# Kernel optimization log

Hardware: AMD Instinct MI355X
Metric: run time of the kernel (lower is better)

Reference implementation:

```python
import jax, jax.numpy as jnp
import numpy as np

EMBED_DIM = 1024
ATTN_DIM = 128
B, S = 4, 2048


def setup_inputs() -> dict:
    key = jax.random.key(0)
    k1, k2, k3, k4 = jax.random.split(key, 4)
    embedded = jax.random.normal(k1, (B, S, EMBED_DIM), dtype=jnp.float32)
    # torch nn.Linear weights are [out_features, in_features]
    scale = 1.0 / np.sqrt(EMBED_DIM)
    Wk = jax.random.uniform(k2, (ATTN_DIM, EMBED_DIM), dtype=jnp.float32, minval=-scale, maxval=scale)
    Wq = jax.random.uniform(k3, (ATTN_DIM, EMBED_DIM), dtype=jnp.float32, minval=-scale, maxval=scale)
    Wv = jax.random.uniform(k4, (ATTN_DIM, EMBED_DIM), dtype=jnp.float32, minval=-scale, maxval=scale)
    return {"embedded": embedded, "Wk": Wk, "Wq": Wq, "Wv": Wv}


def reference(embedded, Wk, Wq, Wv):
    # projections (no bias): x @ W.T
    k = jnp.einsum('bse,ae->bsa', embedded, Wk)  # [B,S,A]
    q = jnp.einsum('bse,ae->bsa', embedded, Wq)
    v = jnp.einsum('bse,ae->bsa', embedded, Wv)
    ad = k.shape[-1]
    scores = jnp.einsum('bqa,bka->bqk', q, k) / jnp.sqrt(jnp.float32(ad))  # [B,S,S]
    causal = jnp.tril(jnp.ones((scores.shape[1], scores.shape[1]), dtype=bool))
    scores = jnp.where(causal, scores, -jnp.inf)
    probs = jax.nn.softmax(scores, axis=-1)
    out = jnp.einsum('bqk,bka->bqa', probs, v)
    return jnp.round(out, 4)
```

## Files before the change

kernel.cpp:

```cpp
#include <hip/hip_runtime.h>
#include <hip/hip_bf16.h>
#include <math.h>

#define B 4
#define S 2048
#define E 1024
#define A 128
#define CHUNK 256
#define NCHMAX 8

typedef __attribute__((ext_vector_type(8))) short short8;
typedef __attribute__((ext_vector_type(4))) float floatx4;

static __device__ __forceinline__ short f2bf(float f) {
  union { float f; unsigned u; } c;
  c.f = f;
  unsigned r = (c.u + 0x7fffu + ((c.u >> 16) & 1u)) >> 16;
  return (short)r;
}
static __device__ __forceinline__ unsigned f2bf2(float x, float y) {
  __hip_bfloat162 h = __float22bfloat162_rn(float2{x, y});
  union { __hip_bfloat162 h; unsigned u; } c;
  c.h = h;
  return c.u;
}

__global__ __launch_bounds__(256) void wconv(
    const float* __restrict__ Wq,
    const float* __restrict__ Wk,
    const float* __restrict__ Wv,
    short* __restrict__ Wbf) {
  const int which = blockIdx.y;
  const float* Wp = (which == 0) ? Wq : (which == 1) ? Wk : Wv;
  short* o = Wbf + (size_t)which * A * E;
  const int f = blockIdx.x * 256 + threadIdx.x;
  const float4 v = *(const float4*)&Wp[(size_t)f * 4];
  uint2 p; p.x = f2bf2(v.x, v.y); p.y = f2bf2(v.z, v.w);
  *(uint2*)&o[(size_t)f * 4] = p;
}

#define PJ 72
__global__ __launch_bounds__(256) void proj_gemm(
    const float* __restrict__ X,
    const short* __restrict__ Wbf,
    short* __restrict__ Qbf,
    short* __restrict__ Kbf,
    short* __restrict__ Vt) {
  __shared__ short As[64 * PJ];
  __shared__ short Bs[128 * PJ];

  const int m0 = blockIdx.x * 64;
  const int which = blockIdx.y;
  const short* Wpb = Wbf + (size_t)which * A * E;

  const int tid = threadIdx.x;
  const int wave = tid >> 6;
  const int lane = tid & 63;
  const int mh = wave & 1;
  const int nh = wave >> 1;
  const int l16 = lane & 15;
  const int quad = lane >> 4;

  int arow[4], ac4[4], brow[4], bc8[4];
#pragma unroll
  for (int i = 0; i < 4; ++i) {
    const int fa = tid + i * 256;
    arow[i] = fa >> 4; ac4[i] = fa & 15;
    const int fb = tid + i * 256;
    brow[i] = fb >> 3; bc8[i] = fb & 7;
  }

  floatx4 acc[2][4] = {};
  float4 aplf[4];
  short8 bplf[4];

#pragma unroll
  for (int i = 0; i < 4; ++i) {
    aplf[i] = *(const float4*)&X[(size_t)(m0 + arow[i]) * E + ac4[i] * 4];
    bplf[i] = *(const short8*)&Wpb[(size_t)brow[i] * E + bc8[i] * 8];
  }

  for (int k0 = 0; k0 < E; k0 += 64) {
    __syncthreads();
#pragma unroll
    for (int i = 0; i < 4; ++i) {
      uint2 p; p.x = f2bf2(aplf[i].x, aplf[i].y); p.y = f2bf2(aplf[i].z, aplf[i].w);
      *(uint2*)&As[arow[i] * PJ + ac4[i] * 4] = p;
      *(short8*)&Bs[brow[i] * PJ + bc8[i] * 8] = bplf[i];
    }
    __syncthreads();

    if (k0 + 64 < E) {
#pragma unroll
      for (int i = 0; i < 4; ++i) {
        aplf[i] = *(const float4*)&X[(size_t)(m0 + arow[i]) * E + (k0 + 64) + ac4[i] * 4];
        bplf[i] = *(const short8*)&Wpb[(size_t)brow[i] * E + (k0 + 64) + bc8[i] * 8];
      }
    }

    short8 afr[2][2], bfr[4][2];
#pragma unroll
    for (int ms = 0; ms < 2; ++ms)
#pragma unroll
      for (int ks = 0; ks < 2; ++ks)
        afr[ms][ks] = *(const short8*)&As[(mh * 32 + ms * 16 + l16) * PJ + ks * 32 + quad * 8];
#pragma unroll
    for (int nt = 0; nt < 4; ++nt)
#pragma unroll
      for (int ks = 0; ks < 2; ++ks)
        bfr[nt][ks] = *(const short8*)&Bs[(nh * 64 + nt * 16 + l16) * PJ + ks * 32 + quad * 8];

#pragma unroll
    for (int ms = 0; ms < 2; ++ms)
#pragma unroll
      for (int nt = 0; nt < 4; ++nt)
#pragma unroll
        for (int ks = 0; ks < 2; ++ks)
          acc[ms][nt] = __builtin_amdgcn_mfma_f32_16x16x32_bf16(
              afr[ms][ks], bfr[nt][ks], acc[ms][nt], 0, 0, 0);
  }

  const float qscale = 0.08838834764831845f;
#pragma unroll
  for (int ms = 0; ms < 2; ++ms) {
#pragma unroll
    for (int nt = 0; nt < 4; ++nt) {
      const int n = nh * 64 + nt * 16 + l16;
      const int mbase = m0 + mh * 32 + ms * 16 + quad * 4;
      if (which == 2) {
        const int b = mbase >> 11, s = mbase & (S - 1);
        short4 p;
        p.x = f2bf(acc[ms][nt][0]); p.y = f2bf(acc[ms][nt][1]);
        p.z = f2bf(acc[ms][nt][2]); p.w = f2bf(acc[ms][nt][3]);
        *(short4*)&Vt[((size_t)b * A + n) * S + s] = p;
      } else {
        short* Outp = (which == 0) ? Qbf : Kbf;
        const float sc = (which == 0) ? qscale : 1.0f;
#pragma unroll
        for (int r = 0; r < 4; ++r)
          Outp[(size_t)(mbase + r) * A + n] = f2bf(acc[ms][nt][r] * sc);
      }
    }
  }
}

#define LK 132
#define LV 68
__global__ __launch_bounds__(256) void attn_part(
    const short* __restrict__ Qbf,
    const short* __restrict__ Kbf,
    const short* __restrict__ Vt,
    float* __restrict__ Opart,
    float* __restrict__ Lpart) {
  __shared__ short Ks[64 * LK];
  __shared__ short Vs[128 * LV];
  __shared__ short Ps[4][16 * LV];

  const int rev = (int)gridDim.x - 1 - (int)blockIdx.x;
  const int qt = rev >> 3;
  const int chunk = rev & 7;
  const int b = qt >> 5;
  const int q0 = (qt & 31) << 6;
  const int nk = q0 + 64;
  const int kstart = chunk * CHUNK;
  if (kstart >= nk) return;
  const int kend = min(kstart + CHUNK, nk);

  const int tid = threadIdx.x;
  const int wave = tid >> 6;
  const int lane = tid & 63;
  const int l16 = lane & 15;
  const int quad = lane >> 4;

  int krow[4], kc8[4], vrow[4], vc8[4];
#pragma unroll
  for (int i = 0; i < 4; ++i) {
    const int f = tid + i * 256;
    krow[i] = f >> 4; kc8[i] = f & 15;
    vrow[i] = f >> 3; vc8[i] = f & 7;
  }

  short8 qfr[4];
  {
    const size_t qrow = (size_t)(b * S + q0 + wave * 16 + l16);
#pragma unroll
    for (int ks = 0; ks < 4; ++ks)
      qfr[ks] = *(const short8*)&Qbf[qrow * A + ks * 32 + quad * 8];
  }

  float l_acc[4] = {0.f, 0.f, 0.f, 0.f};
  floatx4 oacc[8] = {};

  const int myrow = q0 + wave * 16 + quad * 4;
  const short* Kbase = Kbf + (size_t)b * S * A;
  const short* Vbase = Vt + (size_t)b * A * S;

  short8 kplf[4], vplf[4];
#pragma unroll
  for (int i = 0; i < 4; ++i) {
    kplf[i] = *(const short8*)&Kbase[(size_t)(kstart + krow[i]) * A + kc8[i] * 8];
    vplf[i] = *(const short8*)&Vbase[(size_t)vrow[i] * S + kstart + vc8[i] * 8];
  }

  for (int j0 = kstart; j0 < kend; j0 += 64) {
    __syncthreads();
#pragma unroll
    for (int i = 0; i < 4; ++i) {
      *(short8*)&Ks[krow[i] * LK + kc8[i] * 8] = kplf[i];
      *(short8*)&Vs[vrow[i] * LV + vc8[i] * 8] = vplf[i];
    }
    __syncthreads();

    if (j0 + 64 < kend) {
#pragma unroll
      for (int i = 0; i < 4; ++i) {
        kplf[i] = *(const short8*)&Kbase[(size_t)(j0 + 64 + krow[i]) * A + kc8[i] * 8];
        vplf[i] = *(const short8*)&Vbase[(size_t)vrow[i] * S + j0 + 64 + vc8[i] * 8];
      }
    }

    floatx4 sc[4];
#pragma unroll
    for (int nt = 0; nt < 4; ++nt) {
      floatx4 c = {};
#pragma unroll
      for (int ks = 0; ks < 4; ++ks) {
        const short8 bfr = *(const short8*)&Ks[(nt * 16 + l16) * LK + ks * 32 + quad * 8];
        c = __builtin_amdgcn_mfma_f32_16x16x32_bf16(qfr[ks], bfr, c, 0, 0, 0);
      }
      sc[nt] = c;
    }

#pragma unroll
    for (int nt = 0; nt < 4; ++nt) {
      const int key = j0 + nt * 16 + l16;
#pragma unroll
      for (int r = 0; r < 4; ++r) {
        const float p = (key > myrow + r) ? 0.f : __expf(sc[nt][r]);
        sc[nt][r] = p;
        l_acc[r] += p;
      }
    }

#pragma unroll
    for (int nt = 0; nt < 4; ++nt)
#pragma unroll
      for (int r = 0; r < 4; ++r)
        Ps[wave][(quad * 4 + r) * LV + nt * 16 + l16] = f2bf(sc[nt][r]);

    short8 pfr[2];
#pragma unroll
    for (int ks = 0; ks < 2; ++ks)
      pfr[ks] = *(const short8*)&Ps[wave][l16 * LV + ks * 32 + quad * 8];

#pragma unroll
    for (int nt = 0; nt < 8; ++nt) {
#pragma unroll
      for (int ks = 0; ks < 2; ++ks) {
        const short8 vfr = *(const short8*)&Vs[(nt * 16 + l16) * LV + ks * 32 + quad * 8];
        oacc[nt] = __builtin_amdgcn_mfma_f32_16x16x32_bf16(pfr[ks], vfr, oacc[nt], 0, 0, 0);
      }
    }
  }

  const int slot = qt * NCHMAX + chunk;
  float* op = Opart + (size_t)slot * 64 * 128;
  const int lr = wave * 16 + quad * 4;
#pragma unroll
  for (int nt = 0; nt < 8; ++nt)
#pragma unroll
    for (int r = 0; r < 4; ++r)
      op[(lr + r) * 128 + nt * 16 + l16] = oacc[nt][r];

#pragma unroll
  for (int r = 0; r < 4; ++r) {
    float l = l_acc[r];
    l += __shfl_xor(l, 1);
    l += __shfl_xor(l, 2);
    l += __shfl_xor(l, 4);
    l += __shfl_xor(l, 8);
    if (l16 == 0) Lpart[slot * 64 + lr + r] = l;
  }
}

__global__ __launch_bounds__(256) void attn_reduce(
    const float* __restrict__ Opart,
    const float* __restrict__ Lpart,
    float* __restrict__ Out) {
  const int qt = blockIdx.x;
  const int b = qt >> 5;
  const int q0 = (qt & 31) << 6;
  const int nch = (q0 + 64 + CHUNK - 1) / CHUNK;

  const int tid = threadIdx.x;
  const int lr = tid >> 2;
  const int c0 = (tid & 3) * 32;

  float ltot = 0.f;
  for (int c = 0; c < nch; ++c) ltot += Lpart[(qt * NCHMAX + c) * 64 + lr];
  const float inv = 1.f / ltot;

  float4 acc[8] = {};
  for (int c = 0; c < nch; ++c) {
    const float4* op = (const float4*)
        (Opart + ((size_t)(qt * NCHMAX + c) * 64 + lr) * 128 + c0);
#pragma unroll
    for (int i = 0; i < 8; ++i) {
      const float4 v = op[i];
      acc[i].x += v.x; acc[i].y += v.y; acc[i].z += v.z; acc[i].w += v.w;
    }
  }

  float4* o = (float4*)(Out + (size_t)(b * S + q0 + lr) * A + c0);
#pragma unroll
  for (int i = 0; i < 8; ++i) {
    float4 v = acc[i];
    v.x *= inv; v.y *= inv; v.z *= inv; v.w *= inv;
    o[i] = v;
  }
}

extern "C" void kernel_launch(void* const* d_in, const int* in_sizes, int n_in,
                              void* d_out, int out_size, void* d_ws, size_t ws_size,
                              hipStream_t stream) {
  const float* X  = (const float*)d_in[0];
  const float* Wk = (const float*)d_in[1];
  const float* Wq = (const float*)d_in[2];
  const float* Wv = (const float*)d_in[3];
  float* Out = (float*)d_out;

  const size_t qkv_elems = (size_t)B * S * A;
  short* Qbf = (short*)d_ws;
  short* Kbf = Qbf + qkv_elems;
  short* Vt  = Kbf + qkv_elems;
  float* Opart = (float*)(Vt + qkv_elems);
  float* Lpart = Opart + (size_t)1024 * 64 * 128;
  short* Wbf = (short*)(Lpart + (size_t)1024 * 64);

  wconv<<<dim3(A * E / 4 / 256, 3), 256, 0, stream>>>(Wq, Wk, Wv, Wbf);
  dim3 pgrid(B * S / 64, 3);
  proj_gemm<<<pgrid, 256, 0, stream>>>(X, Wbf, Qbf, Kbf, Vt);
  attn_part<<<(B * S / 64) * NCHMAX, 256, 0, stream>>>(Qbf, Kbf, Vt, Opart, Lpart);
  attn_reduce<<<B * S / 64, 256, 0, stream>>>(Opart, Lpart, Out);
}
```

Before: 129.9 us.

## XOR-swizzle LDS tiles, double-prefetch projection loads, split reduce blocks

Replaces padded LDS row strides with XOR-swizzled unpadded layouts for the projection GEMM tiles and the attention K/V tiles, aiming to avoid bank conflicts while using less shared memory. The projection GEMM now keeps two register prefetch buffers in flight, loading two K-steps ahead to hide global latency. Address arithmetic is precomputed outside the loops. The reduce kernel launches twice as many blocks, each handling half the rows, to improve occupancy. The extra prefetch buffers raise register pressure in the projection kernel.

```diff
diff --git a/kernel.cpp b/kernel.cpp
--- a/kernel.cpp
+++ b/kernel.cpp
@@ -39,15 +39,14 @@
   *(uint2*)&o[(size_t)f * 4] = p;
 }
 
-#define PJ 72
 __global__ __launch_bounds__(256) void proj_gemm(
     const float* __restrict__ X,
     const short* __restrict__ Wbf,
     short* __restrict__ Qbf,
     short* __restrict__ Kbf,
     short* __restrict__ Vt) {
-  __shared__ short As[64 * PJ];
-  __shared__ short Bs[128 * PJ];
+  __shared__ short As[64 * 64];
+  __shared__ short Bs[128 * 64];
 
   const int m0 = blockIdx.x * 64;
   const int which = blockIdx.y;
@@ -61,64 +60,74 @@
   const int l16 = lane & 15;
   const int quad = lane >> 4;
 
-  int arow[4], ac4[4], brow[4], bc8[4];
+  int xbase[4], wbase[4], aoff[4], boff[4];
 #pragma unroll
   for (int i = 0; i < 4; ++i) {
     const int fa = tid + i * 256;
-    arow[i] = fa >> 4; ac4[i] = fa & 15;
+    const int arow = fa >> 4, ac4 = fa & 15;
+    xbase[i] = (m0 + arow) * E + ac4 * 4;
+    aoff[i] = arow * 64 + (((ac4 >> 1) ^ (arow & 7)) << 3) + ((ac4 & 1) << 2);
     const int fb = tid + i * 256;
-    brow[i] = fb >> 3; bc8[i] = fb & 7;
-  }
+    const int brow = fb >> 3, bc8 = fb & 7;
+    wbase[i] = brow * E + bc8 * 8;
+    boff[i] = brow * 64 + ((bc8 ^ (brow & 7)) << 3);
+  }
+
+  int arb[2], brb[4], swz[2];
+#pragma unroll
+  for (int ms = 0; ms < 2; ++ms) arb[ms] = (mh * 32 + ms * 16 + l16) * 64;
+#pragma unroll
+  for (int nt = 0; nt < 4; ++nt) brb[nt] = (nh * 64 + nt * 16 + l16) * 64;
+#pragma unroll
+  for (int ks = 0; ks < 2; ++ks) swz[ks] = (((ks * 4 + quad) ^ (l16 & 7)) << 3);
 
   floatx4 acc[2][4] = {};
-  float4 aplf[4];
-  short8 bplf[4];
-
-#pragma unroll
-  for (int i = 0; i < 4; ++i) {
-    aplf[i] = *(const float4*)&X[(size_t)(m0 + arow[i]) * E + ac4[i] * 4];
-    bplf[i] = *(const short8*)&Wpb[(size_t)brow[i] * E + bc8[i] * 8];
-  }
-
-  for (int k0 = 0; k0 < E; k0 += 64) {
-    __syncthreads();
-#pragma unroll
-    for (int i = 0; i < 4; ++i) {
-      uint2 p; p.x = f2bf2(aplf[i].x, aplf[i].y); p.y = f2bf2(aplf[i].z, aplf[i].w);
-      *(uint2*)&As[arow[i] * PJ + ac4[i] * 4] = p;
-      *(short8*)&Bs[brow[i] * PJ + bc8[i] * 8] = bplf[i];
-    }
-    __syncthreads();
-
-    if (k0 + 64 < E) {
-#pragma unroll
-      for (int i = 0; i < 4; ++i) {
-        aplf[i] = *(const float4*)&X[(size_t)(m0 + arow[i]) * E + (k0 + 64) + ac4[i] * 4];
-        bplf[i] = *(const short8*)&Wpb[(size_t)brow[i] * E + (k0 + 64) + bc8[i] * 8];
-      }
-    }
-
-    short8 afr[2][2], bfr[4][2];
-#pragma unroll
-    for (int ms = 0; ms < 2; ++ms)
-#pragma unroll
-      for (int ks = 0; ks < 2; ++ks)
-        afr[ms][ks] = *(const short8*)&As[(mh * 32 + ms * 16 + l16) * PJ + ks * 32 + quad * 8];
-#pragma unroll
-    for (int nt = 0; nt < 4; ++nt)
-#pragma unroll
-      for (int ks = 0; ks < 2; ++ks)
-        bfr[nt][ks] = *(const short8*)&Bs[(nh * 64 + nt * 16 + l16) * PJ + ks * 32 + quad * 8];
-
-#pragma unroll
-    for (int ms = 0; ms < 2; ++ms)
-#pragma unroll
-      for (int nt = 0; nt < 4; ++nt)
-#pragma unroll
-        for (int ks = 0; ks < 2; ++ks)
-          acc[ms][nt] = __builtin_amdgcn_mfma_f32_16x16x32_bf16(
-              afr[ms][ks], bfr[nt][ks], acc[ms][nt], 0, 0, 0);
-  }
+  float4 apl0[4], apl1[4];
+  short8 bpl0[4], bpl1[4];
+
+#pragma unroll
+  for (int i = 0; i < 4; ++i) {
+    apl0[i] = *(const float4*)&X[xbase[i]];
+    bpl0[i] = *(const short8*)&Wpb[wbase[i]];
+    apl1[i] = *(const float4*)&X[xbase[i] + 64];
+    bpl1[i] = *(const short8*)&Wpb[wbase[i] + 64];
+  }
+
+#define PROJ_BODY(APL, BPL, KNEXT)                                            \
+  do {                                                                        \
+    __syncthreads();                                                          \
+    _Pragma("unroll") for (int i = 0; i < 4; ++i) {                           \
+      uint2 pk; pk.x = f2bf2(APL[i].x, APL[i].y);                             \
+      pk.y = f2bf2(APL[i].z, APL[i].w);                                       \
+      *(uint2*)&As[aoff[i]] = pk;                                             \
+      *(short8*)&Bs[boff[i]] = BPL[i];                                        \
+    }                                                                         \
+    __syncthreads();                                                          \
+    if ((KNEXT) < E) {                                                        \
+      _Pragma("unroll") for (int i = 0; i < 4; ++i) {                         \
+        APL[i] = *(const float4*)&X[xbase[i] + (KNEXT)];                      \
+        BPL[i] = *(const short8*)&Wpb[wbase[i] + (KNEXT)];                    \
+      }                                                                       \
+    }                                                                         \
+    short8 afr[2][2], bfr[4][2];                                              \
+    _Pragma("unroll") for (int ms = 0; ms < 2; ++ms)                          \
+      _Pragma("unroll") for (int ks = 0; ks < 2; ++ks)                        \
+        afr[ms][ks] = *(const short8*)&As[arb[ms] + swz[ks]];                 \
+    _Pragma("unroll") for (int nt = 0; nt < 4; ++nt)                          \
+      _Pragma("unroll") for (int ks = 0; ks < 2; ++ks)                        \
+        bfr[nt][ks] = *(const short8*)&Bs[brb[nt] + swz[ks]];                 \
+    _Pragma("unroll") for (int ms = 0; ms < 2; ++ms)                          \
+      _Pragma("unroll") for (int nt = 0; nt < 4; ++nt)                        \
+        _Pragma("unroll") for (int ks = 0; ks < 2; ++ks)                      \
+          acc[ms][nt] = __builtin_amdgcn_mfma_f32_16x16x32_bf16(              \
+              afr[ms][ks], bfr[nt][ks], acc[ms][nt], 0, 0, 0);                \
+  } while (0)
+
+  for (int k0 = 0; k0 < E; k0 += 128) {
+    PROJ_BODY(apl0, bpl0, k0 + 128);
+    PROJ_BODY(apl1, bpl1, k0 + 192);
+  }
+#undef PROJ_BODY
 
   const float qscale = 0.08838834764831845f;
 #pragma unroll
@@ -144,17 +153,16 @@
   }
 }
 
-#define LK 132
-#define LV 68
+#define LP 68
 __global__ __launch_bounds__(256) void attn_part(
     const short* __restrict__ Qbf,
     const short* __restrict__ Kbf,
     const short* __restrict__ Vt,
     float* __restrict__ Opart,
     float* __restrict__ Lpart) {
-  __shared__ short Ks[64 * LK];
-  __shared__ short Vs[128 * LV];
-  __shared__ short Ps[4][16 * LV];
+  __shared__ short Ks[64 * 128];
+  __shared__ short Vs[128 * 64];
+  __shared__ short Ps[4][16 * LP];
 
   const int rev = (int)gridDim.x - 1 - (int)blockIdx.x;
   const int qt = rev >> 3;
@@ -172,13 +180,21 @@
   const int l16 = lane & 15;
   const int quad = lane >> 4;
 
-  int krow[4], kc8[4], vrow[4], vc8[4];
+  int kgb[4], vgb[4], kwoff[4], vwoff[4];
 #pragma unroll
   for (int i = 0; i < 4; ++i) {
     const int f = tid + i * 256;
-    krow[i] = f >> 4; kc8[i] = f & 15;
-    vrow[i] = f >> 3; vc8[i] = f & 7;
-  }
+    const int krow = f >> 4, kc8 = f & 15;
+    kgb[i] = krow * A + kc8 * 8;
+    kwoff[i] = krow * 128 + ((kc8 ^ (krow & 7)) << 3);
+    const int vrow = f >> 3, vc8 = f & 7;
+    vgb[i] = vrow * S + vc8 * 8;
+    vwoff[i] = vrow * 64 + ((vc8 ^ (vrow & 7)) << 3);
+  }
+
+  int swz[4];
+#pragma unroll
+  for (int ks = 0; ks < 4; ++ks) swz[ks] = (((ks * 4 + quad) ^ (l16 & 7)) << 3);
 
   short8 qfr[4];
   {
@@ -198,24 +214,24 @@
   short8 kplf[4], vplf[4];
 #pragma unroll
   for (int i = 0; i < 4; ++i) {
-    kplf[i] = *(const short8*)&Kbase[(size_t)(kstart + krow[i]) * A + kc8[i] * 8];
-    vplf[i] = *(const short8*)&Vbase[(size_t)vrow[i] * S + kstart + vc8[i] * 8];
+    kplf[i] = *(const short8*)&Kbase[kstart * A + kgb[i]];
+    vplf[i] = *(const short8*)&Vbase[vgb[i] + kstart];
   }
 
   for (int j0 = kstart; j0 < kend; j0 += 64) {
     __syncthreads();
 #pragma unroll
     for (int i = 0; i < 4; ++i) {
-      *(short8*)&Ks[krow[i] * LK + kc8[i] * 8] = kplf[i];
-      *(short8*)&Vs[vrow[i] * LV + vc8[i] * 8] = vplf[i];
+      *(short8*)&Ks[kwoff[i]] = kplf[i];
+      *(short8*)&Vs[vwoff[i]] = vplf[i];
     }
     __syncthreads();
 
     if (j0 + 64 < kend) {
 #pragma unroll
       for (int i = 0; i < 4; ++i) {
-        kplf[i] = *(const short8*)&Kbase[(size_t)(j0 + 64 + krow[i]) * A + kc8[i] * 8];
-        vplf[i] = *(const short8*)&Vbase[(size_t)vrow[i] * S + j0 + 64 + vc8[i] * 8];
+        kplf[i] = *(const short8*)&Kbase[(j0 + 64) * A + kgb[i]];
+        vplf[i] = *(const short8*)&Vbase[vgb[i] + j0 + 64];
       }
     }
 
@@ -225,7 +241,7 @@
       floatx4 c = {};
 #pragma unroll
       for (int ks = 0; ks < 4; ++ks) {
-        const short8 bfr = *(const short8*)&Ks[(nt * 16 + l16) * LK + ks * 32 + quad * 8];
+        const short8 bfr = *(const short8*)&Ks[(nt * 16 + l16) * 128 + swz[ks]];
         c = __builtin_amdgcn_mfma_f32_16x16x32_bf16(qfr[ks], bfr, c, 0, 0, 0);
       }
       sc[nt] = c;
@@ -246,18 +262,18 @@
     for (int nt = 0; nt < 4; ++nt)
 #pragma unroll
       for (int r = 0; r < 4; ++r)
-        Ps[wave][(quad * 4 + r) * LV + nt * 16 + l16] = f2bf(sc[nt][r]);
+        Ps[wave][(quad * 4 + r) * LP + nt * 16 + l16] = f2bf(sc[nt][r]);
 
     short8 pfr[2];
 #pragma unroll
     for (int ks = 0; ks < 2; ++ks)
-      pfr[ks] = *(const short8*)&Ps[wave][l16 * LV + ks * 32 + quad * 8];
+      pfr[ks] = *(const short8*)&Ps[wave][l16 * LP + ks * 32 + quad * 8];
 
 #pragma unroll
     for (int nt = 0; nt < 8; ++nt) {
 #pragma unroll
       for (int ks = 0; ks < 2; ++ks) {
-        const short8 vfr = *(const short8*)&Vs[(nt * 16 + l16) * LV + ks * 32 + quad * 8];
+        const short8 vfr = *(const short8*)&Vs[(nt * 16 + l16) * 64 + swz[ks]];
         oacc[nt] = __builtin_amdgcn_mfma_f32_16x16x32_bf16(pfr[ks], vfr, oacc[nt], 0, 0, 0);
       }
     }
@@ -287,25 +303,26 @@
     const float* __restrict__ Opart,
     const float* __restrict__ Lpart,
     float* __restrict__ Out) {
-  const int qt = blockIdx.x;
+  const int qt = blockIdx.x >> 1;
+  const int half = blockIdx.x & 1;
   const int b = qt >> 5;
   const int q0 = (qt & 31) << 6;
   const int nch = (q0 + 64 + CHUNK - 1) / CHUNK;
 
   const int tid = threadIdx.x;
-  const int lr = tid >> 2;
-  const int c0 = (tid & 3) * 32;
+  const int lr = half * 32 + (tid >> 3);
+  const int c0 = (tid & 7) * 16;
 
   float ltot = 0.f;
   for (int c = 0; c < nch; ++c) ltot += Lpart[(qt * NCHMAX + c) * 64 + lr];
   const float inv = 1.f / ltot;
 
-  float4 acc[8] = {};
+  float4 acc[4] = {};
   for (int c = 0; c < nch; ++c) {
     const float4* op = (const float4*)
         (Opart + ((size_t)(qt * NCHMAX + c) * 64 + lr) * 128 + c0);
 #pragma unroll
-    for (int i = 0; i < 8; ++i) {
+    for (int i = 0; i < 4; ++i) {
       const float4 v = op[i];
       acc[i].x += v.x; acc[i].y += v.y; acc[i].z += v.z; acc[i].w += v.w;
     }
@@ -313,7 +330,7 @@
 
   float4* o = (float4*)(Out + (size_t)(b * S + q0 + lr) * A + c0);
 #pragma unroll
-  for (int i = 0; i < 8; ++i) {
+  for (int i = 0; i < 4; ++i) {
     float4 v = acc[i];
     v.x *= inv; v.y *= inv; v.z *= inv; v.w *= inv;
     o[i] = v;
@@ -341,5 +358,5 @@
   dim3 pgrid(B * S / 64, 3);
   proj_gemm<<<pgrid, 256, 0, stream>>>(X, Wbf, Qbf, Kbf, Vt);
   attn_part<<<(B * S / 64) * NCHMAX, 256, 0, stream>>>(Qbf, Kbf, Vt, Opart, Lpart);
-  attn_reduce<<<B * S / 64, 256, 0, stream>>>(Opart, Lpart, Out);
-}
+  attn_reduce<<<B * S / 64 * 2, 256, 0, stream>>>(Opart, Lpart, Out);
+}
```

After: 120.5 us. 1.08x faster.
